# Kernel optimization log

Hardware: AMD Instinct MI355X
Metric: run time of the kernel (lower is better)

The kernel has to match this reference:

```python
import jax, jax.numpy as jnp
import numpy as np

B, T, F, H, D = 64, 256, 128, 8, 256
E = F * H          # MHA embed dim = input_dim * feat_dim = 1024
HEADS = 4
HD = E // HEADS


def setup_inputs() -> dict:
    key = jax.random.key(0)
    ks = jax.random.split(key, 12)
    def w(k, shape, fan_in):
        return (jax.random.normal(k, shape, jnp.float32) / np.float32(np.sqrt(fan_in)))
    z = lambda *s: jnp.zeros(s, jnp.float32)
    return {
        "x": jax.random.normal(ks[0], (B, T, F), jnp.float32),
        # input_attn MLP: Linear(F, F//4) -> GELU -> Linear(F//4, F) -> Sigmoid
        "attn_w1": w(ks[1], (F, F // 4), F), "attn_b1": z(F // 4),
        "attn_w2": w(ks[2], (F // 4, F), F // 4), "attn_b2": z(F),
        # bank of F tiny GRUs (input=1, hidden=H), stacked along feature axis
        "W_ih": w(ks[3], (F, 3 * H), 1),        # input weight per feature (input size 1)
        "W_hh": w(ks[4], (F, 3 * H, H), H),
        "b_ih": z(F, 3 * H), "b_hh": z(F, 3 * H),
        # MultiheadAttention(E, 4 heads)
        "in_proj_w": w(ks[5], (E, 3 * E), E), "in_proj_b": z(3 * E),
        "mha_out_w": w(ks[6], (E, E), E), "mha_out_b": z(E),
        # out_proj: Linear(E, D)
        "outp_w": w(ks[7], (E, D), E), "outp_b": z(D),
        # FFN: Linear(D, 2D) -> GELU -> Linear(2D, D)
        "ffn_w1": w(ks[8], (D, 2 * D), D), "ffn_b1": z(2 * D),
        "ffn_w2": w(ks[9], (2 * D, D), 2 * D), "ffn_b2": z(D),
    }


def _forward(x, attn_w1, attn_b1, attn_w2, attn_b2,
             W_ih, W_hh, b_ih, b_hh,
             in_proj_w, in_proj_b, mha_out_w, mha_out_b,
             outp_w, outp_b, ffn_w1, ffn_b1, ffn_w2, ffn_b2):
    gelu = lambda v: jax.nn.gelu(v, approximate=False)
    bs, ts, _ = x.shape
    # feature gating (dropout layers are identity in eval mode)
    input_attn = jax.nn.sigmoid(gelu(x @ attn_w1 + attn_b1) @ attn_w2 + attn_b2)  # [B,T,F]
    xg = x * input_attn

    # fused bank of F independent GRUs (input size 1, hidden H), scanned over time
    def step(h, xt):  # h: [B,F,H], xt: [B,F]
        gi = xt[..., None] * W_ih + b_ih                       # [B,F,3H]
        gh = jnp.einsum('bfh,fgh->bfg', h, W_hh) + b_hh        # [B,F,3H]
        ir, iz, inn = jnp.split(gi, 3, axis=-1)
        hr, hz, hn = jnp.split(gh, 3, axis=-1)
        r = jax.nn.sigmoid(ir + hr)
        zg = jax.nn.sigmoid(iz + hz)
        n = jnp.tanh(inn + r * hn)
        h_new = (1.0 - zg) * n + zg * h
        return h_new, h_new

    h0 = jnp.zeros((bs, F, H), x.dtype)
    _, ys = jax.lax.scan(step, h0, jnp.moveaxis(xg, 1, 0))     # ys: [T,B,F,H]
    out = jnp.moveaxis(ys, 0, 1).reshape(bs, ts, E)            # [B,T,E]

    # self-attention (eval: no dropout)
    qkv = out @ in_proj_w + in_proj_b                          # [B,T,3E]
    q, k, v = jnp.split(qkv, 3, axis=-1)
    hsplit = lambda t: t.reshape(bs, ts, HEADS, HD)
    q, k, v = hsplit(q), hsplit(k), hsplit(v)
    scores = jnp.einsum('bqhd,bkhd->bhqk', q, k) / np.float32(np.sqrt(HD))
    attn = jax.nn.softmax(scores, axis=-1)
    ctx = jnp.einsum('bhqk,bkhd->bqhd', attn, v).reshape(bs, ts, E)
    mha_out = ctx @ mha_out_w + mha_out_b

    h1 = mha_out @ outp_w + outp_b                             # [B,T,D]
    ffn = gelu(h1 @ ffn_w1 + ffn_b1) @ ffn_w2 + ffn_b2
    y = h1 + ffn
    feature_importance = input_attn.sum(-1)                    # [B,T]
    return y, feature_importance, input_attn


def reference(x, attn_w1, attn_b1, attn_w2, attn_b2,
              W_ih, W_hh, b_ih, b_hh,
              in_proj_w, in_proj_b, mha_out_w, mha_out_b,
              outp_w, outp_b, ffn_w1, ffn_b1, ffn_w2, ffn_b2):
    return _forward(x, attn_w1, attn_b1, attn_w2, attn_b2,
                    W_ih, W_hh, b_ih, b_hh,
                    in_proj_w, in_proj_b, mha_out_w, mha_out_b,
                    outp_w, outp_b, ffn_w1, ffn_b1, ffn_w2, ffn_b2)
```

## Files before the change

### kernel.cpp

```cpp
#include <hip/hip_runtime.h>
#include <hip/hip_bf16.h>
#include <math.h>

#define B_  64
#define T_  256
#define F_  128
#define H_  8
#define E_  1024
#define NH_ 4
#define HD_ 256
#define D_  256

#define OFF_Y_  0L
#define OFF_FI_ 4194304L
#define OFF_IA_ 4210688L

typedef unsigned short u16;
typedef unsigned int   u32;
typedef short bf16x8 __attribute__((ext_vector_type(8)));
typedef float f32x4  __attribute__((ext_vector_type(4)));

__device__ __forceinline__ float bf2f(u16 u) {
  union { u32 u; float f; } x; x.u = ((u32)u) << 16; return x.f;
}
__device__ __forceinline__ u16 f2bf(float f) {
  union { float f; u32 u; } x; x.f = f;
  u32 r = (x.u + 0x7fffu + ((x.u >> 16) & 1u)) >> 16;
  return (u16)r;
}
__device__ __forceinline__ float gelu_exact(float v) {
  return 0.5f * v * (1.f + erff(v * 0.70710678118654752f));
}
__device__ __forceinline__ float sigmoidf_(float v) {
  return 1.f / (1.f + __expf(-v));
}
__device__ __forceinline__ float ldv(const void* p, long i, bool isf) {
  return isf ? ((const float*)p)[i] : bf2f(((const u16*)p)[i]);
}
__device__ __forceinline__ void stv(void* p, long i, float v, bool isf) {
  if (isf) ((float*)p)[i] = v;
  else ((u16*)p)[i] = f2bf(v);
}
__device__ __forceinline__ void gld16(void* lds, const void* g) {
  __builtin_amdgcn_global_load_lds(
      (const __attribute__((address_space(1))) u32*)g,
      (__attribute__((address_space(3))) u32*)lds, 16, 0, 0);
}

__global__ void detect_dtype(const u16* __restrict__ x, u32* __restrict__ flag) {
  if (threadIdx.x == 0 && blockIdx.x == 0) {
    int good = 0;
    for (int i = 0; i < 512; ++i) {
      u16 v = x[i];
      int e = (v >> 7) & 0xFF;
      if (v == 0 || (e >= 100 && e <= 140)) ++good;
    }
    *flag = (good >= 450) ? 0u : 1u;
  }
}

__global__ __launch_bounds__(256)
void convert_in(const void* __restrict__ src, u16* __restrict__ dst, int n,
                const u32* __restrict__ flag) {
  const bool isf = (*flag != 0);
  int i = blockIdx.x * 256 + threadIdx.x;
  if (i < n) dst[i] = isf ? f2bf(((const float*)src)[i]) : ((const u16*)src)[i];
}

__global__ void transpose_cvt(const void* __restrict__ in, u16* __restrict__ out,
                              int R, int C, const u32* __restrict__ flag) {
  const bool isf = (*flag != 0);
  __shared__ float t[32][33];
  const int c0 = blockIdx.x * 32, r0 = blockIdx.y * 32;
  const int tx = threadIdx.x, ty = threadIdx.y;
  for (int i = ty; i < 32; i += 8)
    t[i][tx] = ldv(in, (long)(r0 + i) * C + c0 + tx, isf);
  __syncthreads();
  for (int i = ty; i < 32; i += 8)
    out[(long)(c0 + i) * R + r0 + tx] = f2bf(t[tx][i]);
}

__global__ __launch_bounds__(128)
void input_mlp2(const void* __restrict__ x,
                const void* __restrict__ w1, const void* __restrict__ b1,
                const void* __restrict__ w2, const void* __restrict__ b2,
                const u32* __restrict__ flag,
                u16* __restrict__ xg, void* __restrict__ dout) {
  const bool isf = (*flag != 0);
  const long row = blockIdx.x;
  const int tid = threadIdx.x;
  __shared__ float xr[F_];
  __shared__ float hid[32];
  __shared__ float red[2];
  float xv = ldv(x, row * F_ + tid, isf);
  xr[tid] = xv;
  __syncthreads();
  if (tid < 32) {
    float s = ldv(b1, tid, isf);
    for (int f = 0; f < F_; ++f) s += xr[f] * ldv(w1, f * 32 + tid, isf);
    hid[tid] = gelu_exact(s);
  }
  __syncthreads();
  float s = ldv(b2, tid, isf);
  #pragma unroll 8
  for (int j = 0; j < 32; ++j) s += hid[j] * ldv(w2, j * F_ + tid, isf);
  float ia = sigmoidf_(s);
  stv(dout, OFF_IA_ + row * F_ + tid, ia, isf);
  xg[row * F_ + tid] = f2bf(ia * xv);
  float v = ia;
  for (int o = 32; o > 0; o >>= 1) v += __shfl_down(v, o);
  if ((tid & 63) == 0) red[tid >> 6] = v;
  __syncthreads();
  if (tid == 0) stv(dout, OFF_FI_ + row, red[0] + red[1], isf);
}

__global__ __launch_bounds__(256)
void gru_scan4(const u16* __restrict__ xg, const void* __restrict__ W_ih,
               const void* __restrict__ W_hh, const void* __restrict__ b_ih,
               const void* __restrict__ b_hh, const u32* __restrict__ flag,
               u16* __restrict__ gruo) {
  const bool isf = (*flag != 0);
  const int tid = threadIdx.x;
  const int ric = tid >> 3;
  const int j   = tid & 7;
  const int rec = blockIdx.x * 32 + ric;
  const int b = rec >> 7, f = rec & 127;
  __shared__ __align__(16) float hbuf[32][8];
  float whr[8], whz[8], whn[8];
  #pragma unroll
  for (int k = 0; k < 8; ++k) {
    whr[k] = ldv(W_hh, (long)f * 192 + j * 8 + k, isf);
    whz[k] = ldv(W_hh, (long)f * 192 + (8 + j) * 8 + k, isf);
    whn[k] = ldv(W_hh, (long)f * 192 + (16 + j) * 8 + k, isf);
  }
  const float wir = ldv(W_ih, f * 24 + j, isf);
  const float wiz = ldv(W_ih, f * 24 + 8 + j, isf);
  const float win = ldv(W_ih, f * 24 + 16 + j, isf);
  const float cbr = ldv(b_ih, f * 24 + j, isf) + ldv(b_hh, f * 24 + j, isf);
  const float cbz = ldv(b_ih, f * 24 + 8 + j, isf) + ldv(b_hh, f * 24 + 8 + j, isf);
  const float bin_ = ldv(b_ih, f * 24 + 16 + j, isf);
  const float bhn_ = ldv(b_hh, f * 24 + 16 + j, isf);
  float h[8];
  #pragma unroll
  for (int k = 0; k < 8; ++k) h[k] = 0.f;
  const u16* xp = xg + (long)b * T_ * F_ + f;
  u16* op = gruo + (long)b * T_ * E_ + f * 8 + j;
  float xv = bf2f(xp[0]);
  for (int t = 0; t < T_; ++t) {
    float xn = (t + 1 < T_) ? bf2f(xp[(t + 1) * F_]) : 0.f;
    float ar = fmaf(xv, wir, cbr);
    float az = fmaf(xv, wiz, cbz);
    float an = bhn_;
    #pragma unroll
    for (int k = 0; k < 8; ++k) {
      ar = fmaf(h[k], whr[k], ar);
      az = fmaf(h[k], whz[k], az);
      an = fmaf(h[k], whn[k], an);
    }
    const float r = sigmoidf_(ar);
    const float z = sigmoidf_(az);
    const float a = fmaf(r, an, fmaf(xv, win, bin_));
    const float e = __expf(2.f * a);
    const float n = 1.f - 2.f / (e + 1.f);
    const float hn = fmaf(z, h[j] - n, n);
    op[(long)t * E_] = f2bf(hn);
    hbuf[ric][j] = hn;
    f32x4 h0 = *(const f32x4*)&hbuf[ric][0];
    f32x4 h1 = *(const f32x4*)&hbuf[ric][4];
    h[0] = h0[0]; h[1] = h0[1]; h[2] = h0[2]; h[3] = h0[3];
    h[4] = h1[0]; h[5] = h1[1]; h[6] = h1[2]; h[7] = h1[3];
    xv = xn;
  }
}

template <int EPI, int COUT>
__global__ __launch_bounds__(256)
void gemm_bt(const u16* __restrict__ A, int lda,
             const u16* __restrict__ Bp, int ldb,
             void* __restrict__ Cg, int ldc,
             const u16* __restrict__ bias, const u16* __restrict__ resid,
             int K, int nbm, const u32* __restrict__ flag) {
  const bool isf = (*flag != 0);
  const int bm = blockIdx.x % nbm, bn = blockIdx.x / nbm;
  const int w = threadIdx.x >> 6, lane = threadIdx.x & 63;
  __shared__ __align__(16) u16 As[128 * 64];
  __shared__ __align__(16) u16 Bs[128 * 64];
  const long m0 = (long)bm * 128, n0 = (long)bn * 128;
  const int wm = w >> 1, wn = w & 1;
  const int lr8 = lane >> 3;
  const int csw = ((lane & 7) ^ (lr8 & 7)) * 8;
  f32x4 acc[4][4] = {};
  const int nk = K >> 6;
  const int lr = lane & 15, lq = lane >> 4;
  for (int kt = 0; kt < nk; ++kt) {
    const int k0 = kt << 6;
    __syncthreads();
    #pragma unroll
    for (int c = 0; c < 4; ++c) {
      const int rb = w * 32 + c * 8;
      gld16((char*)As + rb * 128, A + (m0 + rb + lr8) * (long)lda + k0 + csw);
      gld16((char*)Bs + rb * 128, Bp + (n0 + rb + lr8) * (long)ldb + k0 + csw);
    }
    __syncthreads();
    #pragma unroll
    for (int sub = 0; sub < 2; ++sub) {
      const int ch = sub * 4 + lq;
      const int co = ((ch ^ (lr & 7)) << 3);
      bf16x8 af[4], bfv[4];
      #pragma unroll
      for (int i = 0; i < 4; ++i)
        af[i] = *(const bf16x8*)&As[(wm * 64 + i * 16 + lr) * 64 + co];
      #pragma unroll
      for (int i = 0; i < 4; ++i)
        bfv[i] = *(const bf16x8*)&Bs[(wn * 64 + i * 16 + lr) * 64 + co];
      #pragma unroll
      for (int i = 0; i < 4; ++i) {
        #pragma unroll
        for (int j = 0; j < 4; ++j)
          acc[i][j] = __builtin_amdgcn_mfma_f32_16x16x32_bf16(af[i], bfv[j], acc[i][j], 0, 0, 0);
      }
    }
  }
  const int rq = lq * 4;
  #pragma unroll
  for (int j = 0; j < 4; ++j) {
    const long col = n0 + wn * 64 + j * 16 + lr;
    const float bv = (EPI >= 1) ? bf2f(bias[col]) : 0.f;
    #pragma unroll
    for (int i = 0; i < 4; ++i) {
      const long row0 = m0 + wm * 64 + i * 16 + rq;
      #pragma unroll
      for (int q = 0; q < 4; ++q) {
        const long row = row0 + q;
        float v = acc[i][j][q] + bv;
        if (EPI == 2) v = gelu_exact(v);
        if (EPI == 3) v += bf2f(resid[row * (long)ldc + col]);
        if (COUT) stv(Cg, row * (long)ldc + col, v, isf);
        else ((u16*)Cg)[row * (long)ldc + col] = f2bf(v);
      }
    }
  }
}

__global__ __launch_bounds__(256)
void attn_fused(const u16* __restrict__ qkv, u16* __restrict__ ctx) {
  const int z = blockIdx.y, bb = z >> 2, hh = z & 3;
  const int w = threadIdx.x >> 6, lane = threadIdx.x & 63;
  const int tid = threadIdx.x;
  const long t0 = (long)blockIdx.x * 64;
  __shared__ __align__(16) u16 P1[10240];
  __shared__ __align__(16) u16 Pl[64 * 264];
  __shared__ __align__(16) u16 Vt[256 * 40];
  const u16* qb = qkv + (long)bb * T_ * 3 * E_ + hh * HD_;
  const u16* kb = qb + E_;
  const u16* vb = qb + 2 * E_;
  const int rr = lane >> 2, cc = lane & 3;
  const int lr = lane & 15, lq = lane >> 4, lk = lq * 8;
  f32x4 acc[16] = {};
  for (int kt = 0; kt < 8; ++kt) {
    const int k0 = kt * 32;
    __syncthreads();
    gld16((char*)P1 + w * 16 * 64, qb + (t0 + w * 16 + rr) * (3L * E_) + k0 + cc * 8);
    #pragma unroll
    for (int c = 0; c < 4; ++c) {
      const int rb = w * 64 + c * 16;
      gld16((char*)P1 + 4096 + rb * 64, kb + (long)(rb + rr) * (3L * E_) + k0 + cc * 8);
    }
    __syncthreads();
    bf16x8 aq = *(const bf16x8*)&P1[(w * 16 + lr) * 32 + lk];
    #pragma unroll
    for (int nt = 0; nt < 16; ++nt) {
      bf16x8 bk = *(const bf16x8*)&P1[2048 + (nt * 16 + lr) * 32 + lk];
      acc[nt] = __builtin_amdgcn_mfma_f32_16x16x32_bf16(aq, bk, acc[nt], 0, 0, 0);
    }
  }
  #pragma unroll
  for (int q = 0; q < 4; ++q) {
    float mx = -3.4e38f;
    #pragma unroll
    for (int nt = 0; nt < 16; ++nt) mx = fmaxf(mx, acc[nt][q]);
    mx = fmaxf(mx, __shfl_xor(mx, 1));
    mx = fmaxf(mx, __shfl_xor(mx, 2));
    mx = fmaxf(mx, __shfl_xor(mx, 4));
    mx = fmaxf(mx, __shfl_xor(mx, 8));
    float e[16], sum = 0.f;
    #pragma unroll
    for (int nt = 0; nt < 16; ++nt) {
      e[nt] = __expf((acc[nt][q] - mx) * 0.0625f);
      sum += e[nt];
    }
    sum += __shfl_xor(sum, 1);
    sum += __shfl_xor(sum, 2);
    sum += __shfl_xor(sum, 4);
    sum += __shfl_xor(sum, 8);
    const float inv = 1.f / sum;
    const int rowl = w * 16 + lq * 4 + q;
    #pragma unroll
    for (int nt = 0; nt < 16; ++nt)
      Pl[rowl * 264 + nt * 16 + lr] = f2bf(e[nt] * inv);
  }
  f32x4 acc2[16] = {};
  for (int st = 0; st < 8; ++st) {
    const int s0 = st * 32;
    __syncthreads();
    #pragma unroll
    for (int c = 0; c < 4; ++c) {
      const int rb = w * 8 + c * 2;
      gld16((char*)P1 + rb * 512, vb + (s0 + rb + (lane >> 5)) * (3L * E_) + (lane & 31) * 8);
    }
    __syncthreads();
    u16 col[32];
    #pragma unroll
    for (int si = 0; si < 32; ++si) col[si] = P1[si * 256 + tid];
    #pragma unroll
    for (int cq = 0; cq < 4; ++cq)
      *(uint4*)&Vt[tid * 40 + cq * 8] = *(const uint4*)&col[cq * 8];
    __syncthreads();
    bf16x8 pa = *(const bf16x8*)&Pl[(w * 16 + lr) * 264 + s0 + lk];
    #pragma unroll
    for (int nt = 0; nt < 16; ++nt) {
      bf16x8 bv = *(const bf16x8*)&Vt[(nt * 16 + lr) * 40 + lk];
      acc2[nt] = __builtin_amdgcn_mfma_f32_16x16x32_bf16(pa, bv, acc2[nt], 0, 0, 0);
    }
  }
  const int rq = lq * 4;
  #pragma unroll
  for (int nt = 0; nt < 16; ++nt) {
    const int col = nt * 16 + lr;
    #pragma unroll
    for (int q = 0; q < 4; ++q) {
      const long row = t0 + w * 16 + rq + q;
      ctx[((long)bb * T_ + row) * E_ + hh * HD_ + col] = f2bf(acc2[nt][q]);
    }
  }
}

extern "C" void kernel_launch(void* const* d_in, const int* in_sizes, int n_in,
                              void* d_out, int out_size, void* d_ws, size_t ws_size,
                              hipStream_t stream) {
  (void)in_sizes; (void)n_in; (void)out_size; (void)ws_size;
  char* ws = (char*)d_ws;
  u16* BIASA = (u16*)(ws + 0);
  u32* FLAG  = (u32*)(ws + 12288);
  u16* wtI   = (u16*)(ws + 65536);
  u16* wtM   = (u16*)(ws + 6356992);
  u16* wtO   = (u16*)(ws + 8454144);
  u16* wtF1  = (u16*)(ws + 8978432);
  u16* wtF2  = (u16*)(ws + 9240576);
  u16* XG    = (u16*)(ws + 9502720);
  u16* GRUO  = (u16*)(ws + 16777216);
  u16* CTX   = GRUO;
  u16* QKV   = (u16*)(ws + 50331648);
  u16* MHA   = (u16*)(ws + 50331648);
  u16* H1    = (u16*)(ws + 83886080);
  u16* FFH   = (u16*)(ws + 92274688);

  detect_dtype<<<1, 64, 0, stream>>>((const u16*)d_in[0], FLAG);

  convert_in<<<12, 256, 0, stream>>>(d_in[10], BIASA + 0,    3072, FLAG);
  convert_in<<<4,  256, 0, stream>>>(d_in[12], BIASA + 3072, 1024, FLAG);
  convert_in<<<1,  256, 0, stream>>>(d_in[14], BIASA + 4096, 256,  FLAG);
  convert_in<<<2,  256, 0, stream>>>(d_in[16], BIASA + 4352, 512,  FLAG);
  convert_in<<<1,  256, 0, stream>>>(d_in[18], BIASA + 4864, 256,  FLAG);

  dim3 tb(32, 8);
  transpose_cvt<<<dim3(3072 / 32, 1024 / 32), tb, 0, stream>>>(d_in[9],  wtI,  1024, 3072, FLAG);
  transpose_cvt<<<dim3(1024 / 32, 1024 / 32), tb, 0, stream>>>(d_in[11], wtM,  1024, 1024, FLAG);
  transpose_cvt<<<dim3(256 / 32, 1024 / 32),  tb, 0, stream>>>(d_in[13], wtO,  1024, 256,  FLAG);
  transpose_cvt<<<dim3(512 / 32, 256 / 32),   tb, 0, stream>>>(d_in[15], wtF1, 256,  512,  FLAG);
  transpose_cvt<<<dim3(256 / 32, 512 / 32),   tb, 0, stream>>>(d_in[17], wtF2, 512,  256,  FLAG);

  input_mlp2<<<B_ * T_, 128, 0, stream>>>(d_in[0], d_in[1], d_in[2], d_in[3], d_in[4],
                                          FLAG, XG, d_out);
  gru_scan4<<<256, 256, 0, stream>>>(XG, d_in[5], d_in[6], d_in[7], d_in[8], FLAG, GRUO);

  gemm_bt<1, 0><<<dim3(128 * 24, 1), 256, 0, stream>>>(GRUO, 1024, wtI, 1024,
      QKV, 3072, BIASA, nullptr, 1024, 128, FLAG);
  attn_fused<<<dim3(4, B_ * NH_), 256, 0, stream>>>(QKV, CTX);
  gemm_bt<1, 0><<<dim3(128 * 8, 1), 256, 0, stream>>>(CTX, 1024, wtM, 1024,
      MHA, 1024, BIASA + 3072, nullptr, 1024, 128, FLAG);
  gemm_bt<1, 0><<<dim3(128 * 2, 1), 256, 0, stream>>>(MHA, 1024, wtO, 1024,
      H1, 256, BIASA + 4096, nullptr, 1024, 128, FLAG);
  gemm_bt<2, 0><<<dim3(128 * 4, 1), 256, 0, stream>>>(H1, 256, wtF1, 256,
      FFH, 512, BIASA + 4352, nullptr, 256, 128, FLAG);
  gemm_bt<3, 1><<<dim3(128 * 2, 1), 256, 0, stream>>>(FFH, 512, wtF2, 512,
      d_out, 256, BIASA + 4864, H1, 512, 128, FLAG);
}
```

Baseline: 467.1 us.

## Add double-buffered 256x256 GEMM with XCD remapping for QKV and MHA-out projections

Adds a new 512-thread GEMM kernel with 256x256 output tiles, double-buffered LDS staging via global_load_lds, explicit vmcnt waits and sched barriers to overlap loads with MFMA work. It also remaps block IDs across the 8 XCDs so that neighbouring tiles share L2. The two largest projections (QKV in_proj and the MHA output projection) now use it instead of the 128x128 single-buffered kernel. The larger tiles cut global traffic per FLOP, but with a single block per CU occupancy is lower and the grid has fewer blocks, which can leave CUs unevenly loaded.

```diff
diff --git a/kernel.cpp b/kernel.cpp
--- a/kernel.cpp
+++ b/kernel.cpp
@@ -46,6 +46,12 @@
       (const __attribute__((address_space(1))) u32*)g,
       (__attribute__((address_space(3))) u32*)lds, 16, 0, 0);
 }
+__device__ __forceinline__ void bar_() {
+  __builtin_amdgcn_sched_barrier(0);
+  __builtin_amdgcn_s_barrier();
+  __builtin_amdgcn_sched_barrier(0);
+}
+#define VMCNTN(n) asm volatile("s_waitcnt vmcnt(" #n ")" ::: "memory")
 
 __global__ void detect_dtype(const u16* __restrict__ x, u32* __restrict__ flag) {
   if (threadIdx.x == 0 && blockIdx.x == 0) {
@@ -171,6 +177,90 @@
     h[4] = h1[0]; h[5] = h1[1]; h[6] = h1[2]; h[7] = h1[3];
     xv = xn;
   }
+}
+
+__global__ __launch_bounds__(512, 1)
+void gemm8p(const u16* __restrict__ A, int lda,
+            const u16* __restrict__ Bp, int ldb,
+            u16* __restrict__ Cg, int ldc,
+            const u16* __restrict__ bias,
+            int K, int nbm, int nwg) {
+  const int bid = blockIdx.x;
+  const int q8 = nwg >> 3, r8 = nwg & 7;
+  const int xcd = bid & 7, off = bid >> 3;
+  const int wg = (xcd < r8) ? xcd * (q8 + 1) + off
+                            : r8 * (q8 + 1) + (xcd - r8) * q8 + off;
+  const int bm = wg % nbm, bn = wg / nbm;
+  const long m0 = (long)bm * 256, n0 = (long)bn * 256;
+  const int tid = threadIdx.x;
+  const int wid = tid >> 6, lane = tid & 63;
+  const int wm = wid >> 2, wn = wid & 3;
+  const int lr = lane & 15, lq = lane >> 4;
+  const int co = ((lq ^ ((lr >> 1) & 3)) << 3);
+  __shared__ __align__(16) u16 As[2][2][4096];
+  __shared__ __align__(16) u16 Bs[2][2][4096];
+  const int srow = lane >> 2;
+  const int scsw = (((lane & 3) ^ ((lane >> 3) & 3)) << 3);
+  const u16* Aw = A + (m0 + wid * 16 + srow) * (long)lda + scsw;
+  const u16* Bw = Bp + (n0 + wid * 16 + srow) * (long)ldb + scsw;
+  const long ha = 128L * lda, hb = 128L * ldb;
+
+  f32x4 acc[8][4] = {};
+  const int nk = K >> 5;
+  const int L = (nk >> 1) - 1;
+
+#define STA(d, h, kt) gld16(&As[d][h][wid * 512], Aw + (h) * ha + (kt) * 32)
+#define STB(d, h, kt) gld16(&Bs[d][h][wid * 512], Bw + (h) * hb + (kt) * 32)
+#define RDA(d, ib, v) { _Pragma("unroll") for (int i2 = 0; i2 < 4; ++i2) \
+    v[i2] = *(const bf16x8*)&As[d][wm][((ib) * 16 + i2 * 16 + lr) * 32 + co]; }
+#define RDB(d, v) { _Pragma("unroll") for (int jj = 0; jj < 4; ++jj) \
+    v[jj] = *(const bf16x8*)&Bs[d][wn >> 1][((wn & 1) * 64 + jj * 16 + lr) * 32 + co]; }
+#define MM16(IB, AV, BV) { _Pragma("unroll") for (int i2 = 0; i2 < 4; ++i2) { \
+    _Pragma("unroll") for (int jj = 0; jj < 4; ++jj) \
+      acc[(IB) + i2][jj] = __builtin_amdgcn_mfma_f32_16x16x32_bf16(AV[i2], BV[jj], acc[(IB) + i2][jj], 0, 0, 0); } }
+
+  STA(0, 0, 0); STA(0, 1, 0); STB(0, 0, 0); STB(0, 1, 0);
+  STB(1, 0, 1); STB(1, 1, 1);
+  VMCNTN(2); bar_();
+
+  for (int it = 0; ; ++it) {
+    const int t2 = 2 * it + 2, t3 = 2 * it + 3;
+    const bool more = (it < L);
+    bf16x8 a[4], b[4];
+    RDB(0, b); RDA(0, 0, a);
+    STA(1, 0, t2 - 1); STA(1, 1, t2 - 1);
+    bar_(); MM16(0, a, b); bar_();
+    RDA(0, 4, a);
+    if (more) { STB(0, 0, t2); STB(0, 1, t2); }
+    bar_(); MM16(4, a, b); bar_();
+    if (more) { VMCNTN(2); } else { VMCNTN(0); }
+    RDB(1, b); RDA(1, 0, a);
+    if (more) { STA(0, 0, t2); STA(0, 1, t2); }
+    bar_(); MM16(0, a, b); bar_();
+    RDA(1, 4, a);
+    if (more) { STB(1, 0, t3); STB(1, 1, t3); }
+    bar_(); MM16(4, a, b); bar_();
+    if (!more) break;
+    VMCNTN(2);
+  }
+  #pragma unroll
+  for (int i = 0; i < 8; ++i) {
+    #pragma unroll
+    for (int j = 0; j < 4; ++j) {
+      const long col = n0 + wn * 64 + j * 16 + lr;
+      const float bv = bf2f(bias[col]);
+      #pragma unroll
+      for (int qq = 0; qq < 4; ++qq) {
+        const long row = m0 + wm * 128 + i * 16 + lq * 4 + qq;
+        Cg[row * (long)ldc + col] = f2bf(acc[i][j][qq] + bv);
+      }
+    }
+  }
+#undef STA
+#undef STB
+#undef RDA
+#undef RDB
+#undef MM16
 }
 
 template <int EPI, int COUT>
@@ -205,14 +295,14 @@
     #pragma unroll
     for (int sub = 0; sub < 2; ++sub) {
       const int ch = sub * 4 + lq;
-      const int co = ((ch ^ (lr & 7)) << 3);
+      const int cof = ((ch ^ (lr & 7)) << 3);
       bf16x8 af[4], bfv[4];
       #pragma unroll
       for (int i = 0; i < 4; ++i)
-        af[i] = *(const bf16x8*)&As[(wm * 64 + i * 16 + lr) * 64 + co];
+        af[i] = *(const bf16x8*)&As[(wm * 64 + i * 16 + lr) * 64 + cof];
       #pragma unroll
       for (int i = 0; i < 4; ++i)
-        bfv[i] = *(const bf16x8*)&Bs[(wn * 64 + i * 16 + lr) * 64 + co];
+        bfv[i] = *(const bf16x8*)&Bs[(wn * 64 + i * 16 + lr) * 64 + cof];
       #pragma unroll
       for (int i = 0; i < 4; ++i) {
         #pragma unroll
@@ -326,11 +416,11 @@
   const int rq = lq * 4;
   #pragma unroll
   for (int nt = 0; nt < 16; ++nt) {
-    const int col = nt * 16 + lr;
+    const int cold = nt * 16 + lr;
     #pragma unroll
     for (int q = 0; q < 4; ++q) {
       const long row = t0 + w * 16 + rq + q;
-      ctx[((long)bb * T_ + row) * E_ + hh * HD_ + col] = f2bf(acc2[nt][q]);
+      ctx[((long)bb * T_ + row) * E_ + hh * HD_ + cold] = f2bf(acc2[nt][q]);
     }
   }
 }
@@ -374,11 +464,11 @@
                                           FLAG, XG, d_out);
   gru_scan4<<<256, 256, 0, stream>>>(XG, d_in[5], d_in[6], d_in[7], d_in[8], FLAG, GRUO);
 
-  gemm_bt<1, 0><<<dim3(128 * 24, 1), 256, 0, stream>>>(GRUO, 1024, wtI, 1024,
-      QKV, 3072, BIASA, nullptr, 1024, 128, FLAG);
+  gemm8p<<<dim3(64 * 12), 512, 0, stream>>>(GRUO, 1024, wtI, 1024,
+      QKV, 3072, BIASA, 1024, 64, 64 * 12);
   attn_fused<<<dim3(4, B_ * NH_), 256, 0, stream>>>(QKV, CTX);
-  gemm_bt<1, 0><<<dim3(128 * 8, 1), 256, 0, stream>>>(CTX, 1024, wtM, 1024,
-      MHA, 1024, BIASA + 3072, nullptr, 1024, 128, FLAG);
+  gemm8p<<<dim3(64 * 4), 512, 0, stream>>>(CTX, 1024, wtM, 1024,
+      MHA, 1024, BIASA + 3072, 1024, 64, 64 * 4);
   gemm_bt<1, 0><<<dim3(128 * 2, 1), 256, 0, stream>>>(MHA, 1024, wtO, 1024,
       H1, 256, BIASA + 4096, nullptr, 1024, 128, FLAG);
   gemm_bt<2, 0><<<dim3(128 * 4, 1), 256, 0, stream>>>(H1, 256, wtF1, 256,
```

Result: slower. 494.6 us (+5.9%).
